# Kernel tuning notes

Hardware: AMD Instinct MI355X
Metric: run time of the kernel (lower is better)

Reference implementation:

```python
import jax, jax.numpy as jnp
import numpy as np

NUM_HEADS = 9
NUM_KV_HEADS = 3
HEAD_DIM = 64
ROPE_BASE = 10000.0


def _rope_cos_sin(seq_len, dtype):
    inv_freq = 1.0 / (ROPE_BASE ** (jnp.arange(0, HEAD_DIM, 2, dtype=jnp.float32) / HEAD_DIM))
    t = jnp.arange(seq_len, dtype=jnp.float32)
    freqs = jnp.einsum('s,d->sd', t, inv_freq)            # [S, HEAD_DIM//2]
    emb = jnp.concatenate([freqs, freqs], axis=-1)        # [S, HEAD_DIM]
    return jnp.cos(emb).astype(dtype), jnp.sin(emb).astype(dtype)


def _rotate_half(x):
    x1, x2 = jnp.split(x, 2, axis=-1)
    return jnp.concatenate([-x2, x1], axis=-1)


def setup_inputs() -> dict:
    key = jax.random.key(0)
    ks = jax.random.split(key, 5)
    B, S, H = 4, 2048, 576
    scale = 1.0 / np.sqrt(H)
    return {
        'hidden_states': jax.random.normal(ks[0], (B, S, H), dtype=jnp.float32),
        'Wq': jax.random.normal(ks[1], (H, H), dtype=jnp.float32) * scale,
        'Wk': jax.random.normal(ks[2], (NUM_KV_HEADS * HEAD_DIM, H), dtype=jnp.float32) * scale,
        'Wv': jax.random.normal(ks[3], (NUM_KV_HEADS * HEAD_DIM, H), dtype=jnp.float32) * scale,
        'Wo': jax.random.normal(ks[4], (H, H), dtype=jnp.float32) * scale,
    }


def reference(hidden_states, Wq, Wk, Wv, Wo):
    B, S, H = hidden_states.shape
    groups = NUM_HEADS // NUM_KV_HEADS

    # QKV projections (nn.Linear: x @ W.T), then [B, nH, S, hd]
    q = jnp.einsum('bsh,oh->bso', hidden_states, Wq).reshape(B, S, NUM_HEADS, HEAD_DIM).transpose(0, 2, 1, 3)
    k = jnp.einsum('bsh,oh->bso', hidden_states, Wk).reshape(B, S, NUM_KV_HEADS, HEAD_DIM).transpose(0, 2, 1, 3)
    v = jnp.einsum('bsh,oh->bso', hidden_states, Wv).reshape(B, S, NUM_KV_HEADS, HEAD_DIM).transpose(0, 2, 1, 3)

    # RoPE (position_ids=None path: broadcast over batch and heads)
    cos, sin = _rope_cos_sin(S, hidden_states.dtype)      # [S, hd]
    cos = cos[None, None]
    sin = sin[None, None]
    q = q * cos + _rotate_half(q) * sin
    k = k * cos + _rotate_half(k) * sin

    # GQA: repeat_interleave KV heads over dim=1
    k = jnp.repeat(k, groups, axis=1)                     # [B, nH, S, hd]
    v = jnp.repeat(v, groups, axis=1)

    # Causal SDPA, softmax in fp32 (matches F.scaled_dot_product_attention is_causal=True)
    scores = jnp.einsum('bhqd,bhkd->bhqk', q, k) / np.sqrt(HEAD_DIM)
    causal = jnp.tril(jnp.ones((S, S), dtype=bool))
    scores = jnp.where(causal[None, None], scores, jnp.finfo(jnp.float32).min)
    attn = jax.nn.softmax(scores.astype(jnp.float32), axis=-1).astype(q.dtype)
    out = jnp.einsum('bhqk,bhkd->bhqd', attn, v)          # [B, nH, S, hd]

    out = out.transpose(0, 2, 1, 3).reshape(B, S, H)
    return jnp.einsum('bso,ho->bsh', out, Wo)
```

## Files before the change

### kernel.cpp

```cpp
#include <hip/hip_runtime.h>
#include <stdint.h>
#include <stddef.h>

#define BATCH   4
#define SEQ     2048
#define HDIM    576
#define NHEADS  9
#define NKV     3
#define HD      64
#define GROUPS  3

typedef __bf16 bf16x8 __attribute__((ext_vector_type(8)));
typedef float  f32x4  __attribute__((ext_vector_type(4)));

__device__ __forceinline__ unsigned short f2bf(float f) {
    union { float f; unsigned u; } x; x.f = f;
    unsigned r = (x.u + 0x7FFFu + ((x.u >> 16) & 1u)) >> 16;
    return (unsigned short)r;
}

__device__ __forceinline__ float bf2f(unsigned short us) {
    union { unsigned u; float f; } x; x.u = ((unsigned)us) << 16;
    return x.f;
}

__device__ __forceinline__ f32x4 mfma16(bf16x8 a, bf16x8 b, f32x4 c) {
    return __builtin_amdgcn_mfma_f32_16x16x32_bf16(a, b, c, 0, 0, 0);
}

__global__ void rope_table_kernel(float* __restrict__ cos_t, float* __restrict__ sin_t) {
    int idx = blockIdx.x * blockDim.x + threadIdx.x;
    if (idx >= SEQ * 32) return;
    int s = idx >> 5, i = idx & 31;
    float invf = expf(-(float)i * (9.210340371976184f / 32.0f));
    float ang = (float)s * invf;
    cos_t[idx] = cosf(ang);
    sin_t[idx] = sinf(ang);
}

__launch_bounds__(256, 2)
__global__ void qkv_kernel(const float* __restrict__ x,
                           const float* __restrict__ Wq,
                           const float* __restrict__ Wk,
                           const float* __restrict__ Wv,
                           const float* __restrict__ cos_t,
                           const float* __restrict__ sin_t,
                           unsigned short* __restrict__ qo_ws,
                           unsigned short* __restrict__ k_ws,
                           unsigned short* __restrict__ vT_ws) {
    __shared__ __align__(16) unsigned short aT[2][64][40];
    __shared__ __align__(16) unsigned short bT[64][40];

    const int rt0 = blockIdx.x * 2;
    const int ct = blockIdx.y;
    const int t = threadIdx.x;
    const int w = t >> 6, l = t & 63;
    const int lr = l & 15, lk8 = (l >> 4) * 8;

    const float* W; int wbase;
    if (ct < 9)       { W = Wq; wbase = ct * 64; }
    else if (ct < 12) { W = Wk; wbase = (ct - 9) * 64; }
    else              { W = Wv; wbase = (ct - 12) * 64; }

    const int arow = t >> 2, kg = t & 3;

    f32x4 acc[2][4];
#pragma unroll
    for (int hf = 0; hf < 2; ++hf)
#pragma unroll
        for (int nf = 0; nf < 4; ++nf)
#pragma unroll
            for (int i = 0; i < 4; ++i) acc[hf][nf][i] = 0.0f;

    for (int k0 = 0; k0 < HDIM; k0 += 32) {
        __syncthreads();
#pragma unroll
        for (int hf = 0; hf < 2; ++hf) {
            const float4* ap = reinterpret_cast<const float4*>(
                x + (size_t)((rt0 + hf) * 64 + arow) * HDIM + k0 + kg * 8);
            float4 a0 = ap[0], a1 = ap[1];
            unsigned short* p = &aT[hf][arow][kg * 8];
            p[0] = f2bf(a0.x); p[1] = f2bf(a0.y); p[2] = f2bf(a0.z); p[3] = f2bf(a0.w);
            p[4] = f2bf(a1.x); p[5] = f2bf(a1.y); p[6] = f2bf(a1.z); p[7] = f2bf(a1.w);
        }
        {
            const float4* bp = reinterpret_cast<const float4*>(
                W + (size_t)(wbase + arow) * HDIM + k0 + kg * 8);
            float4 b0 = bp[0], b1 = bp[1];
            unsigned short* p = &bT[arow][kg * 8];
            p[0] = f2bf(b0.x); p[1] = f2bf(b0.y); p[2] = f2bf(b0.z); p[3] = f2bf(b0.w);
            p[4] = f2bf(b1.x); p[5] = f2bf(b1.y); p[6] = f2bf(b1.z); p[7] = f2bf(b1.w);
        }
        __syncthreads();

#pragma unroll
        for (int hf = 0; hf < 2; ++hf) {
            bf16x8 af = *reinterpret_cast<const bf16x8*>(&aT[hf][w * 16 + lr][lk8]);
#pragma unroll
            for (int nf = 0; nf < 4; ++nf) {
                bf16x8 bfr = *reinterpret_cast<const bf16x8*>(&bT[nf * 16 + lr][lk8]);
                acc[hf][nf] = mfma16(af, bfr, acc[hf][nf]);
            }
        }
    }

    const float QSCALE = 0.18033688011112042f;
    const int rowin = w * 16 + (l >> 4) * 4;
#pragma unroll
    for (int hf = 0; hf < 2; ++hf) {
        const int rt = rt0 + hf;
#pragma unroll
        for (int r = 0; r < 4; ++r) {
            const int grow = rt * 64 + rowin + r;
            const int b = grow >> 11, s = grow & 2047;
            if (ct < 12) {
#pragma unroll
                for (int nf = 0; nf < 2; ++nf) {
                    const int d = nf * 16 + lr;
                    const float c  = cos_t[s * 32 + d];
                    const float sn = sin_t[s * 32 + d];
                    const float lo = acc[hf][nf][r];
                    const float hi = acc[hf][nf + 2][r];
                    if (ct < 9) {
                        const size_t base = (size_t)grow * HDIM + ct * 64;
                        qo_ws[base + d]      = f2bf((lo * c - hi * sn) * QSCALE);
                        qo_ws[base + d + 32] = f2bf((hi * c + lo * sn) * QSCALE);
                    } else {
                        const size_t base = (((size_t)(b * NKV + (ct - 9))) * SEQ + s) * HD;
                        k_ws[base + d]      = f2bf(lo * c - hi * sn);
                        k_ws[base + d + 32] = f2bf(hi * c + lo * sn);
                    }
                }
            } else {
                const size_t base = ((size_t)(b * NKV + (ct - 12))) * SEQ * HD;
#pragma unroll
                for (int nf = 0; nf < 4; ++nf)
                    vT_ws[base + (size_t)(nf * 16 + lr) * SEQ + s] = f2bf(acc[hf][nf][r]);
            }
        }
    }
}

__launch_bounds__(256, 2)
__global__ void attn_mfma(unsigned short* __restrict__ qo_ws,
                          const unsigned short* __restrict__ k_ws,
                          const unsigned short* __restrict__ vT_ws) {
    __shared__ __align__(16) unsigned short kT[64][72];
    __shared__ __align__(16) unsigned short vT[64][72];
    __shared__ __align__(16) unsigned short pT[4][16][72];

    const int flat = blockIdx.x + 16 * (blockIdx.y + 9 * blockIdx.z);
    const int wsort = (flat % 8) * 72 + (flat / 8);
    const int g = wsort / 48;
    const int rem = wsort % 48;
    const int b = g / 3, kh = g % 3;
    const int hg = rem / 16, pairi = rem % 16;
    const int h = kh * 3 + hg;

    const int t = threadIdx.x, w = t >> 6, l = t & 63;
    const int lr = l & 15, lk8 = (l >> 4) * 8;

    const size_t kvbase = ((size_t)(b * NKV + kh)) * SEQ * HD;
    const int row = t >> 3, c8 = (t & 7) * 8;
    const int srow_in = w * 16 + (l >> 4) * 4;

    const float THR2 = 11.541560327111708f;

    for (int ph = 0; ph < 2; ++ph) {
        const int qt = ph ? (31 - pairi) : pairi;

        size_t qbase = ((size_t)(b * SEQ + qt * 64 + w * 16 + lr)) * HDIM + h * 64;
        bf16x8 qa[2];
        qa[0] = *reinterpret_cast<const bf16x8*>(&qo_ws[qbase + lk8]);
        qa[1] = *reinterpret_cast<const bf16x8*>(&qo_ws[qbase + 32 + lk8]);

        float m[4] = {-1e30f, -1e30f, -1e30f, -1e30f};
        float suml[4] = {0.f, 0.f, 0.f, 0.f};
        f32x4 oacc[4];
#pragma unroll
        for (int nf = 0; nf < 4; ++nf)
#pragma unroll
            for (int i = 0; i < 4; ++i) oacc[nf][i] = 0.0f;

        uint4 kreg[2], vreg[2];
#pragma unroll
        for (int it = 0; it < 2; ++it) {
            int rr = it * 32 + row;
            kreg[it] = *reinterpret_cast<const uint4*>(&k_ws[kvbase + (size_t)rr * HD + c8]);
            vreg[it] = *reinterpret_cast<const uint4*>(&vT_ws[kvbase + (size_t)rr * SEQ + c8]);
        }
        __syncthreads();
#pragma unroll
        for (int it = 0; it < 2; ++it) {
            int rr = it * 32 + row;
            *reinterpret_cast<uint4*>(&kT[rr][c8]) = kreg[it];
            *reinterpret_cast<uint4*>(&vT[rr][c8]) = vreg[it];
        }
        __syncthreads();

        for (int kt = 0; kt <= qt; ++kt) {
            if (kt < qt) {
#pragma unroll
                for (int it = 0; it < 2; ++it) {
                    int rr = it * 32 + row;
                    kreg[it] = *reinterpret_cast<const uint4*>(
                        &k_ws[kvbase + (size_t)((kt + 1) * 64 + rr) * HD + c8]);
                    vreg[it] = *reinterpret_cast<const uint4*>(
                        &vT_ws[kvbase + (size_t)rr * SEQ + (kt + 1) * 64 + c8]);
                }
            }

            f32x4 sacc[4];
#pragma unroll
            for (int nf = 0; nf < 4; ++nf)
#pragma unroll
                for (int i = 0; i < 4; ++i) sacc[nf][i] = 0.0f;
            __builtin_amdgcn_s_setprio(1);
#pragma unroll
            for (int kf = 0; kf < 2; ++kf) {
#pragma unroll
                for (int nf = 0; nf < 4; ++nf) {
                    bf16x8 bfr = *reinterpret_cast<const bf16x8*>(&kT[nf * 16 + lr][kf * 32 + lk8]);
                    sacc[nf] = mfma16(qa[kf], bfr, sacc[nf]);
                }
            }
            __builtin_amdgcn_s_setprio(0);

            float sv[4][4];
            float lmax[4];
            if (kt == qt) {
#pragma unroll
                for (int r = 0; r < 4; ++r) {
                    int qrow = qt * 64 + srow_in + r;
                    float mx = -1e30f;
#pragma unroll
                    for (int nf = 0; nf < 4; ++nf) {
                        float sc = sacc[nf][r];
                        int kcol = kt * 64 + nf * 16 + lr;
                        if (kcol > qrow) sc = -1e30f;
                        sv[nf][r] = sc;
                        mx = fmaxf(mx, sc);
                    }
                    lmax[r] = mx;
                }
            } else {
#pragma unroll
                for (int r = 0; r < 4; ++r) {
                    float mx = -1e30f;
#pragma unroll
                    for (int nf = 0; nf < 4; ++nf) {
                        float sc = sacc[nf][r];
                        sv[nf][r] = sc;
                        mx = fmaxf(mx, sc);
                    }
                    lmax[r] = mx;
                }
            }

            bool grow = false;
#pragma unroll
            for (int r = 0; r < 4; ++r) grow = grow || (lmax[r] > m[r] + THR2);
            if (__any(grow)) {
#pragma unroll
                for (int r = 0; r < 4; ++r) {
                    float mx = lmax[r];
#pragma unroll
                    for (int off = 1; off < 16; off <<= 1) mx = fmaxf(mx, __shfl_xor(mx, off, 64));
                    float newm = fmaxf(m[r], mx);
                    float corr = exp2f(m[r] - newm);
                    suml[r] *= corr;
#pragma unroll
                    for (int nf = 0; nf < 4; ++nf) oacc[nf][r] *= corr;
                    m[r] = newm;
                }
            }

            float p[4][4];
#pragma unroll
            for (int r = 0; r < 4; ++r) {
#pragma unroll
                for (int nf = 0; nf < 4; ++nf) {
                    float pv = exp2f(sv[nf][r] - m[r]);
                    p[nf][r] = pv;
                    suml[r] += pv;
                }
            }

#pragma unroll
            for (int r = 0; r < 4; ++r)
#pragma unroll
                for (int nf = 0; nf < 4; ++nf)
                    pT[w][(l >> 4) * 4 + r][nf * 16 + lr] = f2bf(p[nf][r]);

            __builtin_amdgcn_s_setprio(1);
#pragma unroll
            for (int kf = 0; kf < 2; ++kf) {
                bf16x8 pa = *reinterpret_cast<const bf16x8*>(&pT[w][lr][kf * 32 + lk8]);
#pragma unroll
                for (int nf = 0; nf < 4; ++nf) {
                    bf16x8 vb = *reinterpret_cast<const bf16x8*>(&vT[nf * 16 + lr][kf * 32 + lk8]);
                    oacc[nf] = mfma16(pa, vb, oacc[nf]);
                }
            }
            __builtin_amdgcn_s_setprio(0);

            if (kt < qt) {
                __syncthreads();
#pragma unroll
                for (int it = 0; it < 2; ++it) {
                    int rr = it * 32 + row;
                    *reinterpret_cast<uint4*>(&kT[rr][c8]) = kreg[it];
                    *reinterpret_cast<uint4*>(&vT[rr][c8]) = vreg[it];
                }
                __syncthreads();
            }
        }

#pragma unroll
        for (int r = 0; r < 4; ++r) {
            float s = suml[r];
#pragma unroll
            for (int off = 1; off < 16; off <<= 1) s += __shfl_xor(s, off, 64);
            float inv = 1.0f / s;
            int srow = qt * 64 + srow_in + r;
            size_t obase = ((size_t)(b * SEQ + srow)) * HDIM + h * 64;
#pragma unroll
            for (int nf = 0; nf < 4; ++nf)
                qo_ws[obase + nf * 16 + lr] = f2bf(oacc[nf][r] * inv);
        }
    }
}

__launch_bounds__(256, 2)
__global__ void oproj_kernel(const unsigned short* __restrict__ o_ws,
                             const float* __restrict__ Wo,
                             float* __restrict__ out) {
    __shared__ __align__(16) unsigned short aT[2][64][40];
    __shared__ __align__(16) unsigned short bT[64][40];

    const int rt0 = blockIdx.x * 2, ct = blockIdx.y;
    const int t = threadIdx.x, w = t >> 6, l = t & 63;
    const int lr = l & 15, lk8 = (l >> 4) * 8;
    const int arow = t >> 2, kg = t & 3;

    f32x4 acc[2][4];
#pragma unroll
    for (int hf = 0; hf < 2; ++hf)
#pragma unroll
        for (int nf = 0; nf < 4; ++nf)
#pragma unroll
            for (int i = 0; i < 4; ++i) acc[hf][nf][i] = 0.0f;

    for (int k0 = 0; k0 < HDIM; k0 += 32) {
        __syncthreads();
#pragma unroll
        for (int hf = 0; hf < 2; ++hf)
            *reinterpret_cast<uint4*>(&aT[hf][arow][kg * 8]) =
                *reinterpret_cast<const uint4*>(
                    &o_ws[(size_t)((rt0 + hf) * 64 + arow) * HDIM + k0 + kg * 8]);
        {
            const float4* bp = reinterpret_cast<const float4*>(
                Wo + (size_t)(ct * 64 + arow) * HDIM + k0 + kg * 8);
            float4 b0 = bp[0], b1 = bp[1];
            unsigned short* p = &bT[arow][kg * 8];
            p[0] = f2bf(b0.x); p[1] = f2bf(b0.y); p[2] = f2bf(b0.z); p[3] = f2bf(b0.w);
            p[4] = f2bf(b1.x); p[5] = f2bf(b1.y); p[6] = f2bf(b1.z); p[7] = f2bf(b1.w);
        }
        __syncthreads();

#pragma unroll
        for (int hf = 0; hf < 2; ++hf) {
            bf16x8 af = *reinterpret_cast<const bf16x8*>(&aT[hf][w * 16 + lr][lk8]);
#pragma unroll
            for (int nf = 0; nf < 4; ++nf) {
                bf16x8 bfr = *reinterpret_cast<const bf16x8*>(&bT[nf * 16 + lr][lk8]);
                acc[hf][nf] = mfma16(af, bfr, acc[hf][nf]);
            }
        }
    }

#pragma unroll
    for (int hf = 0; hf < 2; ++hf)
#pragma unroll
        for (int nf = 0; nf < 4; ++nf)
#pragma unroll
            for (int r = 0; r < 4; ++r) {
                int row = (rt0 + hf) * 64 + w * 16 + (l >> 4) * 4 + r;
                out[(size_t)row * HDIM + ct * 64 + nf * 16 + lr] = acc[hf][nf][r];
            }
}

extern "C" void kernel_launch(void* const* d_in, const int* in_sizes, int n_in,
                              void* d_out, int out_size, void* d_ws, size_t ws_size,
                              hipStream_t stream) {
    const float* x  = (const float*)d_in[0];
    const float* Wq = (const float*)d_in[1];
    const float* Wk = (const float*)d_in[2];
    const float* Wv = (const float*)d_in[3];
    const float* Wo = (const float*)d_in[4];
    float* out = (float*)d_out;

    char* ws = (char*)d_ws;
    float* cos_t = (float*)(ws + 0);
    float* sin_t = (float*)(ws + 262144);
    unsigned short* qo_ws = (unsigned short*)(ws + 524288);
    unsigned short* k_ws  = (unsigned short*)(ws + 9961472);
    unsigned short* vT_ws = (unsigned short*)(ws + 13107200);

    hipLaunchKernelGGL(rope_table_kernel, dim3(256), dim3(256), 0, stream, cos_t, sin_t);
    hipLaunchKernelGGL(qkv_kernel, dim3(64, 15), dim3(256), 0, stream,
                       x, Wq, Wk, Wv, cos_t, sin_t, qo_ws, k_ws, vT_ws);
    hipLaunchKernelGGL(attn_mfma, dim3(16, 9, 4), dim3(256), 0, stream,
                       qo_ws, k_ws, vT_ws);
    hipLaunchKernelGGL(oproj_kernel, dim3(64, 9), dim3(256), 0, stream, qo_ws, Wo, out);
}
```

Before: 172.5 us.

## Process both paired query tiles in one shared K/V sweep

Each attention block used to handle its two balanced query tiles (pairi and 31-pairi) one after the other, streaming K/V tiles from global memory into shared memory separately for each. Now a single loop over key tiles serves both query tiles: tile A is updated while kt <= qtA, and tile B is updated on every iteration. This cuts the redundant global K/V loads and barrier rounds for the shorter tile. The cost is a second set of online-softmax state and output accumulators held in registers, which raises register pressure and could lower occupancy.

```diff
diff --git a/kernel.cpp b/kernel.cpp
--- a/kernel.cpp
+++ b/kernel.cpp
@@ -166,50 +166,55 @@
 
     const float THR2 = 11.541560327111708f;
 
-    for (int ph = 0; ph < 2; ++ph) {
-        const int qt = ph ? (31 - pairi) : pairi;
-
-        size_t qbase = ((size_t)(b * SEQ + qt * 64 + w * 16 + lr)) * HDIM + h * 64;
-        bf16x8 qa[2];
-        qa[0] = *reinterpret_cast<const bf16x8*>(&qo_ws[qbase + lk8]);
-        qa[1] = *reinterpret_cast<const bf16x8*>(&qo_ws[qbase + 32 + lk8]);
-
-        float m[4] = {-1e30f, -1e30f, -1e30f, -1e30f};
-        float suml[4] = {0.f, 0.f, 0.f, 0.f};
-        f32x4 oacc[4];
-#pragma unroll
-        for (int nf = 0; nf < 4; ++nf)
-#pragma unroll
-            for (int i = 0; i < 4; ++i) oacc[nf][i] = 0.0f;
-
-        uint4 kreg[2], vreg[2];
-#pragma unroll
-        for (int it = 0; it < 2; ++it) {
-            int rr = it * 32 + row;
-            kreg[it] = *reinterpret_cast<const uint4*>(&k_ws[kvbase + (size_t)rr * HD + c8]);
-            vreg[it] = *reinterpret_cast<const uint4*>(&vT_ws[kvbase + (size_t)rr * SEQ + c8]);
-        }
-        __syncthreads();
-#pragma unroll
-        for (int it = 0; it < 2; ++it) {
-            int rr = it * 32 + row;
-            *reinterpret_cast<uint4*>(&kT[rr][c8]) = kreg[it];
-            *reinterpret_cast<uint4*>(&vT[rr][c8]) = vreg[it];
-        }
-        __syncthreads();
-
-        for (int kt = 0; kt <= qt; ++kt) {
-            if (kt < qt) {
-#pragma unroll
-                for (int it = 0; it < 2; ++it) {
-                    int rr = it * 32 + row;
-                    kreg[it] = *reinterpret_cast<const uint4*>(
-                        &k_ws[kvbase + (size_t)((kt + 1) * 64 + rr) * HD + c8]);
-                    vreg[it] = *reinterpret_cast<const uint4*>(
-                        &vT_ws[kvbase + (size_t)rr * SEQ + (kt + 1) * 64 + c8]);
-                }
-            }
-
+    const int qtA = pairi;
+    const int qtB = 31 - pairi;
+
+    size_t qbaseA = ((size_t)(b * SEQ + qtA * 64 + w * 16 + lr)) * HDIM + h * 64;
+    size_t qbaseB = ((size_t)(b * SEQ + qtB * 64 + w * 16 + lr)) * HDIM + h * 64;
+    bf16x8 qaA[2], qaB[2];
+    qaA[0] = *reinterpret_cast<const bf16x8*>(&qo_ws[qbaseA + lk8]);
+    qaA[1] = *reinterpret_cast<const bf16x8*>(&qo_ws[qbaseA + 32 + lk8]);
+    qaB[0] = *reinterpret_cast<const bf16x8*>(&qo_ws[qbaseB + lk8]);
+    qaB[1] = *reinterpret_cast<const bf16x8*>(&qo_ws[qbaseB + 32 + lk8]);
+
+    float mA[4], mB[4], sumA[4], sumB[4];
+    f32x4 oaccA[4], oaccB[4];
+#pragma unroll
+    for (int r = 0; r < 4; ++r) { mA[r] = -1e30f; mB[r] = -1e30f; sumA[r] = 0.f; sumB[r] = 0.f; }
+#pragma unroll
+    for (int nf = 0; nf < 4; ++nf)
+#pragma unroll
+        for (int i = 0; i < 4; ++i) { oaccA[nf][i] = 0.0f; oaccB[nf][i] = 0.0f; }
+
+    uint4 kreg[2], vreg[2];
+#pragma unroll
+    for (int it = 0; it < 2; ++it) {
+        int rr = it * 32 + row;
+        kreg[it] = *reinterpret_cast<const uint4*>(&k_ws[kvbase + (size_t)rr * HD + c8]);
+        vreg[it] = *reinterpret_cast<const uint4*>(&vT_ws[kvbase + (size_t)rr * SEQ + c8]);
+    }
+    __syncthreads();
+#pragma unroll
+    for (int it = 0; it < 2; ++it) {
+        int rr = it * 32 + row;
+        *reinterpret_cast<uint4*>(&kT[rr][c8]) = kreg[it];
+        *reinterpret_cast<uint4*>(&vT[rr][c8]) = vreg[it];
+    }
+    __syncthreads();
+
+    for (int kt = 0; kt <= qtB; ++kt) {
+        if (kt < qtB) {
+#pragma unroll
+            for (int it = 0; it < 2; ++it) {
+                int rr = it * 32 + row;
+                kreg[it] = *reinterpret_cast<const uint4*>(
+                    &k_ws[kvbase + (size_t)((kt + 1) * 64 + rr) * HD + c8]);
+                vreg[it] = *reinterpret_cast<const uint4*>(
+                    &vT_ws[kvbase + (size_t)rr * SEQ + (kt + 1) * 64 + c8]);
+            }
+        }
+
+        if (kt <= qtA) {
             f32x4 sacc[4];
 #pragma unroll
             for (int nf = 0; nf < 4; ++nf)
@@ -221,17 +226,16 @@
 #pragma unroll
                 for (int nf = 0; nf < 4; ++nf) {
                     bf16x8 bfr = *reinterpret_cast<const bf16x8*>(&kT[nf * 16 + lr][kf * 32 + lk8]);
-                    sacc[nf] = mfma16(qa[kf], bfr, sacc[nf]);
+                    sacc[nf] = mfma16(qaA[kf], bfr, sacc[nf]);
                 }
             }
             __builtin_amdgcn_s_setprio(0);
 
-            float sv[4][4];
-            float lmax[4];
-            if (kt == qt) {
+            float sv[4][4], lmax[4];
+            if (kt == qtA) {
 #pragma unroll
                 for (int r = 0; r < 4; ++r) {
-                    int qrow = qt * 64 + srow_in + r;
+                    int qrow = qtA * 64 + srow_in + r;
                     float mx = -1e30f;
 #pragma unroll
                     for (int nf = 0; nf < 4; ++nf) {
@@ -259,19 +263,19 @@
 
             bool grow = false;
 #pragma unroll
-            for (int r = 0; r < 4; ++r) grow = grow || (lmax[r] > m[r] + THR2);
+            for (int r = 0; r < 4; ++r) grow = grow || (lmax[r] > mA[r] + THR2);
             if (__any(grow)) {
 #pragma unroll
                 for (int r = 0; r < 4; ++r) {
                     float mx = lmax[r];
 #pragma unroll
                     for (int off = 1; off < 16; off <<= 1) mx = fmaxf(mx, __shfl_xor(mx, off, 64));
-                    float newm = fmaxf(m[r], mx);
-                    float corr = exp2f(m[r] - newm);
-                    suml[r] *= corr;
-#pragma unroll
-                    for (int nf = 0; nf < 4; ++nf) oacc[nf][r] *= corr;
-                    m[r] = newm;
+                    float newm = fmaxf(mA[r], mx);
+                    float corr = exp2f(mA[r] - newm);
+                    sumA[r] *= corr;
+#pragma unroll
+                    for (int nf = 0; nf < 4; ++nf) oaccA[nf][r] *= corr;
+                    mA[r] = newm;
                 }
             }
 
@@ -280,9 +284,9 @@
             for (int r = 0; r < 4; ++r) {
 #pragma unroll
                 for (int nf = 0; nf < 4; ++nf) {
-                    float pv = exp2f(sv[nf][r] - m[r]);
+                    float pv = exp2f(sv[nf][r] - mA[r]);
                     p[nf][r] = pv;
-                    suml[r] += pv;
+                    sumA[r] += pv;
                 }
             }
 
@@ -299,35 +303,142 @@
 #pragma unroll
                 for (int nf = 0; nf < 4; ++nf) {
                     bf16x8 vb = *reinterpret_cast<const bf16x8*>(&vT[nf * 16 + lr][kf * 32 + lk8]);
-                    oacc[nf] = mfma16(pa, vb, oacc[nf]);
+                    oaccA[nf] = mfma16(pa, vb, oaccA[nf]);
                 }
             }
             __builtin_amdgcn_s_setprio(0);
-
-            if (kt < qt) {
-                __syncthreads();
-#pragma unroll
-                for (int it = 0; it < 2; ++it) {
-                    int rr = it * 32 + row;
-                    *reinterpret_cast<uint4*>(&kT[rr][c8]) = kreg[it];
-                    *reinterpret_cast<uint4*>(&vT[rr][c8]) = vreg[it];
-                }
-                __syncthreads();
-            }
-        }
-
-#pragma unroll
-        for (int r = 0; r < 4; ++r) {
-            float s = suml[r];
-#pragma unroll
-            for (int off = 1; off < 16; off <<= 1) s += __shfl_xor(s, off, 64);
-            float inv = 1.0f / s;
-            int srow = qt * 64 + srow_in + r;
-            size_t obase = ((size_t)(b * SEQ + srow)) * HDIM + h * 64;
+        }
+
+        {
+            f32x4 sacc[4];
 #pragma unroll
             for (int nf = 0; nf < 4; ++nf)
-                qo_ws[obase + nf * 16 + lr] = f2bf(oacc[nf][r] * inv);
-        }
+#pragma unroll
+                for (int i = 0; i < 4; ++i) sacc[nf][i] = 0.0f;
+            __builtin_amdgcn_s_setprio(1);
+#pragma unroll
+            for (int kf = 0; kf < 2; ++kf) {
+#pragma unroll
+                for (int nf = 0; nf < 4; ++nf) {
+                    bf16x8 bfr = *reinterpret_cast<const bf16x8*>(&kT[nf * 16 + lr][kf * 32 + lk8]);
+                    sacc[nf] = mfma16(qaB[kf], bfr, sacc[nf]);
+                }
+            }
+            __builtin_amdgcn_s_setprio(0);
+
+            float sv[4][4], lmax[4];
+            if (kt == qtB) {
+#pragma unroll
+                for (int r = 0; r < 4; ++r) {
+                    int qrow = qtB * 64 + srow_in + r;
+                    float mx = -1e30f;
+#pragma unroll
+                    for (int nf = 0; nf < 4; ++nf) {
+                        float sc = sacc[nf][r];
+                        int kcol = kt * 64 + nf * 16 + lr;
+                        if (kcol > qrow) sc = -1e30f;
+                        sv[nf][r] = sc;
+                        mx = fmaxf(mx, sc);
+                    }
+                    lmax[r] = mx;
+                }
+            } else {
+#pragma unroll
+                for (int r = 0; r < 4; ++r) {
+                    float mx = -1e30f;
+#pragma unroll
+                    for (int nf = 0; nf < 4; ++nf) {
+                        float sc = sacc[nf][r];
+                        sv[nf][r] = sc;
+                        mx = fmaxf(mx, sc);
+                    }
+                    lmax[r] = mx;
+                }
+            }
+
+            bool grow = false;
+#pragma unroll
+            for (int r = 0; r < 4; ++r) grow = grow || (lmax[r] > mB[r] + THR2);
+            if (__any(grow)) {
+#pragma unroll
+                for (int r = 0; r < 4; ++r) {
+                    float mx = lmax[r];
+#pragma unroll
+                    for (int off = 1; off < 16; off <<= 1) mx = fmaxf(mx, __shfl_xor(mx, off, 64));
+                    float newm = fmaxf(mB[r], mx);
+                    float corr = exp2f(mB[r] - newm);
+                    sumB[r] *= corr;
+#pragma unroll
+                    for (int nf = 0; nf < 4; ++nf) oaccB[nf][r] *= corr;
+                    mB[r] = newm;
+                }
+            }
+
+            float p[4][4];
+#pragma unroll
+            for (int r = 0; r < 4; ++r) {
+#pragma unroll
+                for (int nf = 0; nf < 4; ++nf) {
+                    float pv = exp2f(sv[nf][r] - mB[r]);
+                    p[nf][r] = pv;
+                    sumB[r] += pv;
+                }
+            }
+
+#pragma unroll
+            for (int r = 0; r < 4; ++r)
+#pragma unroll
+                for (int nf = 0; nf < 4; ++nf)
+                    pT[w][(l >> 4) * 4 + r][nf * 16 + lr] = f2bf(p[nf][r]);
+
+            __builtin_amdgcn_s_setprio(1);
+#pragma unroll
+            for (int kf = 0; kf < 2; ++kf) {
+                bf16x8 pa = *reinterpret_cast<const bf16x8*>(&pT[w][lr][kf * 32 + lk8]);
+#pragma unroll
+                for (int nf = 0; nf < 4; ++nf) {
+                    bf16x8 vb = *reinterpret_cast<const bf16x8*>(&vT[nf * 16 + lr][kf * 32 + lk8]);
+                    oaccB[nf] = mfma16(pa, vb, oaccB[nf]);
+                }
+            }
+            __builtin_amdgcn_s_setprio(0);
+        }
+
+        if (kt < qtB) {
+            __syncthreads();
+#pragma unroll
+            for (int it = 0; it < 2; ++it) {
+                int rr = it * 32 + row;
+                *reinterpret_cast<uint4*>(&kT[rr][c8]) = kreg[it];
+                *reinterpret_cast<uint4*>(&vT[rr][c8]) = vreg[it];
+            }
+            __syncthreads();
+        }
+    }
+
+#pragma unroll
+    for (int r = 0; r < 4; ++r) {
+        float s = sumA[r];
+#pragma unroll
+        for (int off = 1; off < 16; off <<= 1) s += __shfl_xor(s, off, 64);
+        float inv = 1.0f / s;
+        int srow = qtA * 64 + srow_in + r;
+        size_t obase = ((size_t)(b * SEQ + srow)) * HDIM + h * 64;
+#pragma unroll
+        for (int nf = 0; nf < 4; ++nf)
+            qo_ws[obase + nf * 16 + lr] = f2bf(oaccA[nf][r] * inv);
+    }
+#pragma unroll
+    for (int r = 0; r < 4; ++r) {
+        float s = sumB[r];
+#pragma unroll
+        for (int off = 1; off < 16; off <<= 1) s += __shfl_xor(s, off, 64);
+        float inv = 1.0f / s;
+        int srow = qtB * 64 + srow_in + r;
+        size_t obase = ((size_t)(b * SEQ + srow)) * HDIM + h * 64;
+#pragma unroll
+        for (int nf = 0; nf < 4; ++nf)
+            qo_ws[obase + nf * 16 + lr] = f2bf(oaccB[nf][r] * inv);
     }
 }
 
```

Result: faster. 167.9 us (median of 3 runs) (-2.7%).
